# Performance work log

Measured on AMD Instinct MI355X. Metric: run time of the kernel, lower is better.

## Reference

```python
import jax, jax.numpy as jnp
import numpy as np

DEP_NUM, HEAD_NUM, BSZ, DIM, REL = 96, 96, 16, 512, 128


def setup_inputs() -> dict:
    key = jax.random.key(0)
    k1, k2, k3, k4 = jax.random.split(key, 4)
    outs = jax.random.normal(k1, (DEP_NUM, BSZ, DIM), dtype=jnp.float32)
    graph_state = jax.random.normal(k2, (HEAD_NUM, BSZ, DIM), dtype=jnp.float32)
    # nn.init.normal_(std=0.02) for both weights, zero biases
    Wt = 0.02 * jax.random.normal(k3, (DIM, 2 * DIM), dtype=jnp.float32)
    bt = jnp.zeros((DIM,), dtype=jnp.float32)
    Wp = 0.02 * jax.random.normal(k4, (REL, DIM), dtype=jnp.float32)
    bp = jnp.zeros((REL,), dtype=jnp.float32)
    return {"outs": outs, "graph_state": graph_state, "Wt": Wt, "bt": bt, "Wp": Wp, "bp": bp}


def reference(outs, graph_state, Wt, bt, Wp, bp):
    # outs: [dep, b, D], graph_state: [head, b, D]
    # Linear(cat(dep, head)) == dep @ Wt[:, :D].T + head @ Wt[:, D:].T + bt
    D = outs.shape[-1]
    dep_proj = jnp.einsum('dbi,ei->dbe', outs, Wt[:, :D])           # [dep, b, D]
    head_proj = jnp.einsum('hbi,ei->hbe', graph_state, Wt[:, D:])   # [head, b, D]
    # broadcast-sum to pairwise: [dep, b, head, D]
    h = jax.nn.relu(dep_proj[:, :, None, :] + jnp.swapaxes(head_proj, 0, 1)[None] + bt)
    # dropout: identity in eval mode
    scores = jnp.einsum('dbhe,re->dbhr', h, Wp) + bp                # [dep, b, head, REL]
    nil = jnp.zeros(scores.shape[:-1] + (1,), dtype=scores.dtype)
    scores = jnp.concatenate([nil, scores], axis=-1)                # [dep, b, head, REL+1]
    return jax.nn.log_softmax(scores, axis=-1)
```

## Files before the change

### kernel.cpp

```cpp
#include <hip/hip_runtime.h>
#include <hip/hip_bf16.h>
#include <math.h>

#define DEP   96
#define HEADS 96
#define BSZ   16
#define DIM   512
#define REL   128
#define RELP  129

typedef __attribute__((ext_vector_type(8))) short short8;
typedef __attribute__((ext_vector_type(4))) float floatx4;

__device__ __forceinline__ unsigned short f2bf(float x) {
    union { float f; unsigned int u; } c; c.f = x;
    unsigned int r = c.u + 0x7fffu + ((c.u >> 16) & 1u);
    return (unsigned short)(r >> 16);
}

__global__ __launch_bounds__(256) void proj_kernel(
    const float* __restrict__ outs, const float* __restrict__ graph,
    const float* __restrict__ Wt,   const float* __restrict__ bt,
    float* __restrict__ P1, float* __restrict__ P2)
{
    const int z = blockIdx.z;
    const float* A = z ? graph : outs;
    float* C = z ? P2 : P1;
    const int off  = z ? DIM : 0;
    const int row0 = blockIdx.y * 64;
    const int col0 = blockIdx.x * 64;

    __shared__ float As[16][68];
    __shared__ float Bs[16][68];

    const int tid = threadIdx.x;
    const int tx = tid & 15, ty = tid >> 4;
    const int lm = tid >> 2;
    const int lk = (tid & 3) * 4;

    float acc[4][4] = {};

    for (int kt = 0; kt < DIM; kt += 16) {
        float4 av = *(const float4*)(A  + (size_t)(row0 + lm) * DIM       + kt + lk);
        float4 bv = *(const float4*)(Wt + (size_t)(col0 + lm) * (2*DIM) + off + kt + lk);
        As[lk+0][lm] = av.x; As[lk+1][lm] = av.y; As[lk+2][lm] = av.z; As[lk+3][lm] = av.w;
        Bs[lk+0][lm] = bv.x; Bs[lk+1][lm] = bv.y; Bs[lk+2][lm] = bv.z; Bs[lk+3][lm] = bv.w;
        __syncthreads();
        #pragma unroll
        for (int k = 0; k < 16; ++k) {
            float4 a = *(const float4*)&As[k][ty*4];
            float4 b = *(const float4*)&Bs[k][tx*4];
            float aa[4] = {a.x,a.y,a.z,a.w};
            float bb[4] = {b.x,b.y,b.z,b.w};
            #pragma unroll
            for (int i = 0; i < 4; ++i)
                #pragma unroll
                for (int j = 0; j < 4; ++j) acc[i][j] += aa[i]*bb[j];
        }
        __syncthreads();
    }

    #pragma unroll
    for (int i = 0; i < 4; ++i) {
        const int m = row0 + ty*4 + i;
        #pragma unroll
        for (int j = 0; j < 4; ++j) {
            const int n = col0 + tx*4 + j;
            float v = acc[i][j];
            if (!z) v += bt[n];
            C[(size_t)m * DIM + n] = v;
        }
    }
}

__global__ __launch_bounds__(256) void wp_cvt_kernel(
    const float* __restrict__ Wp, unsigned short* __restrict__ WpB)
{
    const int i = blockIdx.x * 256 + threadIdx.x;
    float4 v = *(const float4*)(Wp + (size_t)i * 4);
    ushort4 o;
    o.x = f2bf(v.x); o.y = f2bf(v.y); o.z = f2bf(v.z); o.w = f2bf(v.w);
    *(ushort4*)(WpB + (size_t)i * 4) = o;
}

#define HSS 72
#define WSS 72

__global__ __launch_bounds__(128, 2) void fused_kernel(
    const float* __restrict__ P1, const float* __restrict__ P2,
    const unsigned short* __restrict__ WpB, const float* __restrict__ bp,
    float* __restrict__ out)
{
    const int db = blockIdx.x;
    const int b  = db & 15;

    __shared__ float          drow[DIM];
    __shared__ unsigned short hs[96 * HSS];
    __shared__ unsigned short ws[128 * WSS];

    const int tid  = threadIdx.x;
    const int lane = tid & 63;
    const int wv   = tid >> 6;
    const int ln15 = lane & 15;
    const int quad = lane >> 4;

    #pragma unroll
    for (int q = 0; q < 4; ++q) drow[q*128 + tid] = P1[(size_t)db * DIM + q*128 + tid];
    __syncthreads();

    floatx4 acc[3][8];
    #pragma unroll
    for (int i = 0; i < 3; ++i)
        #pragma unroll
        for (int j = 0; j < 8; ++j) acc[i][j] = (floatx4){0.f,0.f,0.f,0.f};

    for (int kt = 0; kt < DIM; kt += 64) {
        #pragma unroll
        for (int q = 0; q < 12; ++q) {
            const int slot = q*128 + tid;
            const int h  = slot >> 4;
            const int e4 = (slot & 15) * 4;
            float4 p = *(const float4*)(P2 + ((size_t)h * BSZ + b) * DIM + kt + e4);
            float4 d = *(const float4*)&drow[kt + e4];
            ushort4 o;
            o.x = f2bf(fmaxf(p.x + d.x, 0.f));
            o.y = f2bf(fmaxf(p.y + d.y, 0.f));
            o.z = f2bf(fmaxf(p.z + d.z, 0.f));
            o.w = f2bf(fmaxf(p.w + d.w, 0.f));
            *(ushort4*)&hs[h * HSS + e4] = o;
        }
        #pragma unroll
        for (int q = 0; q < 8; ++q) {
            const int slot = q*128 + tid;
            const int r = slot >> 3;
            const int g = (slot & 7) * 8;
            uint4 v = *(const uint4*)(WpB + (size_t)r * DIM + kt + g);
            *(uint4*)&ws[r * WSS + g] = v;
        }
        __syncthreads();

        #pragma unroll
        for (int ks = 0; ks < 64; ks += 32) {
            short8 af[3], bf8[8];
            #pragma unroll
            for (int mt = 0; mt < 3; ++mt)
                af[mt] = *(const short8*)&hs[(wv*48 + mt*16 + ln15) * HSS + ks + quad*8];
            #pragma unroll
            for (int nt = 0; nt < 8; ++nt)
                bf8[nt] = *(const short8*)&ws[(nt*16 + ln15) * WSS + ks + quad*8];
            #pragma unroll
            for (int nt = 0; nt < 8; ++nt)
                #pragma unroll
                for (int mt = 0; mt < 3; ++mt)
                    acc[mt][nt] = __builtin_amdgcn_mfma_f32_16x16x32_bf16(
                        af[mt], bf8[nt], acc[mt][nt], 0, 0, 0);
        }
        __syncthreads();
    }

    float bpv[8];
    #pragma unroll
    for (int nt = 0; nt < 8; ++nt) bpv[nt] = bp[nt*16 + ln15];

    #pragma unroll
    for (int mt = 0; mt < 3; ++mt) {
        #pragma unroll
        for (int reg = 0; reg < 4; ++reg) {
            const int m = wv*48 + mt*16 + quad*4 + reg;
            float s[8];
            float mx = 0.f;
            #pragma unroll
            for (int nt = 0; nt < 8; ++nt) {
                s[nt] = acc[mt][nt][reg] + bpv[nt];
                mx = fmaxf(mx, s[nt]);
            }
            #pragma unroll
            for (int msk = 1; msk < 16; msk <<= 1) mx = fmaxf(mx, __shfl_xor(mx, msk));
            float l = 0.f;
            #pragma unroll
            for (int nt = 0; nt < 8; ++nt) l += __expf(s[nt] - mx);
            #pragma unroll
            for (int msk = 1; msk < 16; msk <<= 1) l += __shfl_xor(l, msk);
            l += __expf(-mx);
            const float lse = mx + __logf(l);

            const size_t base = ((size_t)db * HEADS + m) * RELP;
            #pragma unroll
            for (int nt = 0; nt < 8; ++nt) out[base + 1 + nt*16 + ln15] = s[nt] - lse;
            if (ln15 == 0) out[base] = -lse;
        }
    }
}

extern "C" void kernel_launch(void* const* d_in, const int* in_sizes, int n_in,
                              void* d_out, int out_size, void* d_ws, size_t ws_size,
                              hipStream_t stream) {
    const float* outs  = (const float*)d_in[0];
    const float* graph = (const float*)d_in[1];
    const float* Wt    = (const float*)d_in[2];
    const float* bt    = (const float*)d_in[3];
    const float* Wp    = (const float*)d_in[4];
    const float* bp    = (const float*)d_in[5];
    float* out = (float*)d_out;

    float* P1 = (float*)d_ws;
    float* P2 = P1 + (size_t)DEP * BSZ * DIM;
    unsigned short* WpB = (unsigned short*)(P2 + (size_t)DEP * BSZ * DIM);

    wp_cvt_kernel<<<REL * DIM / (256 * 4), 256, 0, stream>>>(Wp, WpB);
    proj_kernel<<<dim3(DIM/64, (DEP*BSZ)/64, 2), 256, 0, stream>>>(
        outs, graph, Wt, bt, P1, P2);
    fused_kernel<<<DEP*BSZ, 128, 0, stream>>>(P1, P2, WpB, bp, out);
}
```

Measured before the change: 173.7 us.

## Use bf16 MFMA in projection GEMM and store head projection as bf16

```diff
diff --git a/kernel.cpp b/kernel.cpp
--- a/kernel.cpp
+++ b/kernel.cpp
@@ -17,58 +17,82 @@
     unsigned int r = c.u + 0x7fffu + ((c.u >> 16) & 1u);
     return (unsigned short)(r >> 16);
 }
+__device__ __forceinline__ float bflo2f(unsigned int u) {
+    union { unsigned int u; float f; } c; c.u = u << 16; return c.f;
+}
+__device__ __forceinline__ float bfhi2f(unsigned int u) {
+    union { unsigned int u; float f; } c; c.u = u & 0xffff0000u; return c.f;
+}
+
+#define PSS 72
 
 __global__ __launch_bounds__(256) void proj_kernel(
     const float* __restrict__ outs, const float* __restrict__ graph,
     const float* __restrict__ Wt,   const float* __restrict__ bt,
-    float* __restrict__ P1, float* __restrict__ P2)
+    float* __restrict__ P1, unsigned short* __restrict__ P2B)
 {
     const int z = blockIdx.z;
     const float* A = z ? graph : outs;
-    float* C = z ? P2 : P1;
     const int off  = z ? DIM : 0;
     const int row0 = blockIdx.y * 64;
     const int col0 = blockIdx.x * 64;
 
-    __shared__ float As[16][68];
-    __shared__ float Bs[16][68];
-
-    const int tid = threadIdx.x;
-    const int tx = tid & 15, ty = tid >> 4;
-    const int lm = tid >> 2;
-    const int lk = (tid & 3) * 4;
-
-    float acc[4][4] = {};
-
-    for (int kt = 0; kt < DIM; kt += 16) {
-        float4 av = *(const float4*)(A  + (size_t)(row0 + lm) * DIM       + kt + lk);
-        float4 bv = *(const float4*)(Wt + (size_t)(col0 + lm) * (2*DIM) + off + kt + lk);
-        As[lk+0][lm] = av.x; As[lk+1][lm] = av.y; As[lk+2][lm] = av.z; As[lk+3][lm] = av.w;
-        Bs[lk+0][lm] = bv.x; Bs[lk+1][lm] = bv.y; Bs[lk+2][lm] = bv.z; Bs[lk+3][lm] = bv.w;
-        __syncthreads();
-        #pragma unroll
-        for (int k = 0; k < 16; ++k) {
-            float4 a = *(const float4*)&As[k][ty*4];
-            float4 b = *(const float4*)&Bs[k][tx*4];
-            float aa[4] = {a.x,a.y,a.z,a.w};
-            float bb[4] = {b.x,b.y,b.z,b.w};
-            #pragma unroll
-            for (int i = 0; i < 4; ++i)
-                #pragma unroll
-                for (int j = 0; j < 4; ++j) acc[i][j] += aa[i]*bb[j];
-        }
-        __syncthreads();
-    }
-
-    #pragma unroll
-    for (int i = 0; i < 4; ++i) {
-        const int m = row0 + ty*4 + i;
-        #pragma unroll
-        for (int j = 0; j < 4; ++j) {
-            const int n = col0 + tx*4 + j;
-            float v = acc[i][j];
-            if (!z) v += bt[n];
-            C[(size_t)m * DIM + n] = v;
+    __shared__ unsigned short As[64 * PSS];
+    __shared__ unsigned short Ws[64 * PSS];
+
+    const int tid  = threadIdx.x;
+    const int lane = tid & 63;
+    const int wv   = tid >> 6;
+    const int ln15 = lane & 15;
+    const int quad = lane >> 4;
+
+    floatx4 acc[4];
+    #pragma unroll
+    for (int nt = 0; nt < 4; ++nt) acc[nt] = (floatx4){0.f,0.f,0.f,0.f};
+
+    for (int kt = 0; kt < DIM; kt += 64) {
+        #pragma unroll
+        for (int q = 0; q < 4; ++q) {
+            const int slot = q*256 + tid;
+            const int r  = slot >> 4;
+            const int e4 = (slot & 15) * 4;
+            float4 v = *(const float4*)(A + (size_t)(row0 + r) * DIM + kt + e4);
+            ushort4 o;
+            o.x = f2bf(v.x); o.y = f2bf(v.y); o.z = f2bf(v.z); o.w = f2bf(v.w);
+            *(ushort4*)&As[r * PSS + e4] = o;
+        }
+        #pragma unroll
+        for (int q = 0; q < 4; ++q) {
+            const int slot = q*256 + tid;
+            const int r  = slot >> 4;
+            const int e4 = (slot & 15) * 4;
+            float4 v = *(const float4*)(Wt + (size_t)(col0 + r) * (2*DIM) + off + kt + e4);
+            ushort4 o;
+            o.x = f2bf(v.x); o.y = f2bf(v.y); o.z = f2bf(v.z); o.w = f2bf(v.w);
+            *(ushort4*)&Ws[r * PSS + e4] = o;
+        }
+        __syncthreads();
+        #pragma unroll
+        for (int ks = 0; ks < 64; ks += 32) {
+            short8 af = *(const short8*)&As[(wv*16 + ln15) * PSS + ks + quad*8];
+            #pragma unroll
+            for (int nt = 0; nt < 4; ++nt) {
+                short8 bf8 = *(const short8*)&Ws[(nt*16 + ln15) * PSS + ks + quad*8];
+                acc[nt] = __builtin_amdgcn_mfma_f32_16x16x32_bf16(af, bf8, acc[nt], 0, 0, 0);
+            }
+        }
+        __syncthreads();
+    }
+
+    #pragma unroll
+    for (int nt = 0; nt < 4; ++nt) {
+        #pragma unroll
+        for (int reg = 0; reg < 4; ++reg) {
+            const int m = row0 + wv*16 + quad*4 + reg;
+            const int n = col0 + nt*16 + ln15;
+            float v = acc[nt][reg];
+            if (!z) P1[(size_t)m * DIM + n] = v + bt[n];
+            else    P2B[(size_t)m * DIM + n] = f2bf(v);
         }
     }
 }
@@ -87,7 +111,7 @@
 #define WSS 72
 
 __global__ __launch_bounds__(128, 2) void fused_kernel(
-    const float* __restrict__ P1, const float* __restrict__ P2,
+    const float* __restrict__ P1, const unsigned short* __restrict__ P2B,
     const unsigned short* __restrict__ WpB, const float* __restrict__ bp,
     float* __restrict__ out)
 {
@@ -116,18 +140,28 @@
 
     for (int kt = 0; kt < DIM; kt += 64) {
         #pragma unroll
-        for (int q = 0; q < 12; ++q) {
+        for (int q = 0; q < 6; ++q) {
             const int slot = q*128 + tid;
-            const int h  = slot >> 4;
-            const int e4 = (slot & 15) * 4;
-            float4 p = *(const float4*)(P2 + ((size_t)h * BSZ + b) * DIM + kt + e4);
-            float4 d = *(const float4*)&drow[kt + e4];
-            ushort4 o;
-            o.x = f2bf(fmaxf(p.x + d.x, 0.f));
-            o.y = f2bf(fmaxf(p.y + d.y, 0.f));
-            o.z = f2bf(fmaxf(p.z + d.z, 0.f));
-            o.w = f2bf(fmaxf(p.w + d.w, 0.f));
-            *(ushort4*)&hs[h * HSS + e4] = o;
+            const int h  = slot >> 3;
+            const int e8 = (slot & 7) * 8;
+            uint4 pv = *(const uint4*)(P2B + ((size_t)h * BSZ + b) * DIM + kt + e8);
+            float4 d0 = *(const float4*)&drow[kt + e8];
+            float4 d1 = *(const float4*)&drow[kt + e8 + 4];
+            float s0 = fmaxf(bflo2f(pv.x) + d0.x, 0.f);
+            float s1 = fmaxf(bfhi2f(pv.x) + d0.y, 0.f);
+            float s2 = fmaxf(bflo2f(pv.y) + d0.z, 0.f);
+            float s3 = fmaxf(bfhi2f(pv.y) + d0.w, 0.f);
+            float s4 = fmaxf(bflo2f(pv.z) + d1.x, 0.f);
+            float s5 = fmaxf(bfhi2f(pv.z) + d1.y, 0.f);
+            float s6 = fmaxf(bflo2f(pv.w) + d1.z, 0.f);
+            float s7 = fmaxf(bfhi2f(pv.w) + d1.w, 0.f);
+            uint2 o0, o1;
+            o0.x = (unsigned)f2bf(s0) | ((unsigned)f2bf(s1) << 16);
+            o0.y = (unsigned)f2bf(s2) | ((unsigned)f2bf(s3) << 16);
+            o1.x = (unsigned)f2bf(s4) | ((unsigned)f2bf(s5) << 16);
+            o1.y = (unsigned)f2bf(s6) | ((unsigned)f2bf(s7) << 16);
+            *(uint2*)&hs[h * HSS + e8]     = o0;
+            *(uint2*)&hs[h * HSS + e8 + 4] = o1;
         }
         #pragma unroll
         for (int q = 0; q < 8; ++q) {
@@ -204,11 +238,11 @@
     float* out = (float*)d_out;
 
     float* P1 = (float*)d_ws;
-    float* P2 = P1 + (size_t)DEP * BSZ * DIM;
-    unsigned short* WpB = (unsigned short*)(P2 + (size_t)DEP * BSZ * DIM);
+    unsigned short* P2B = (unsigned short*)(P1 + (size_t)DEP * BSZ * DIM);
+    unsigned short* WpB = P2B + (size_t)DEP * BSZ * DIM;
 
     wp_cvt_kernel<<<REL * DIM / (256 * 4), 256, 0, stream>>>(Wp, WpB);
     proj_kernel<<<dim3(DIM/64, (DEP*BSZ)/64, 2), 256, 0, stream>>>(
-        outs, graph, Wt, bt, P1, P2);
-    fused_kernel<<<DEP*BSZ, 128, 0, stream>>>(P1, P2, WpB, bp, out);
-}
+        outs, graph, Wt, bt, P1, P2B);
+    fused_kernel<<<DEP*BSZ, 128, 0, stream>>>(P1, P2B, WpB, bp, out);
+}
```

New measurement: 163.9 us. -5.6%, faster.
